# Optimization experiments

Measured on AMD Instinct MI355X. Metric: run time of the kernel, lower is better.

## Reference

```python
import jax, jax.numpy as jnp
import numpy as np
import math

N_SSM = 64
DIRECTIONS = 4

def setup_inputs() -> dict:
    key = jax.random.key(0)
    ks = jax.random.split(key, 10)
    S, B, E = 1024, 16, 1024
    H, N = DIRECTIONS * N_SSM, 2  # kernel_dim, ndim
    d = {}
    d['x'] = jax.random.normal(ks[0], (S, B, E), jnp.float32)
    for i, name in enumerate(['A_1', 'A_2', 'A_3', 'A_4']):
        d[name] = 0.2 * jax.random.normal(ks[1 + i], (H, N), jnp.float32)
    d['B_1'] = 0.2 * jax.random.normal(ks[5], (H, N), jnp.float32)
    d['B_2'] = 0.2 * jax.random.normal(ks[6], (H, N), jnp.float32)
    d['C_1'] = jax.random.normal(ks[7], (H, N), jnp.float32)
    d['C_2'] = jax.random.normal(ks[8], (H, N), jnp.float32)
    d['omega'] = jax.random.normal(ks[9], (E,), jnp.float32)
    return d


def _compute_kernel(A_1, A_2, A_3, A_4, B_1, B_2, C_1, C_2, Ls):
    # 2D SSM impulse response on an Ls x Ls grid (real, diagonal state dim N).
    # Recurrence (input = delta at (0,0)):
    #   x_h[i,j] = A1*x_h[i,j-1] + A2*x_v[i,j-1] + B1*u[i,j]
    #   x_v[i,j] = A3*x_h[i-1,j] + A4*x_v[i-1,j] + B2*u[i,j]
    #   k[i,j]   = scale*(C1.x_h[i,j] + C2.x_v[i,j])
    H, N = A_1.shape
    scale = math.sqrt(1.0 / N)
    A1, A2 = jax.nn.sigmoid(A_1), jax.nn.sigmoid(A_2)
    A3, A4 = jax.nn.sigmoid(A_3), jax.nn.sigmoid(A_4)
    B1, B2 = jax.nn.sigmoid(B_1), jax.nn.sigmoid(B_2)
    zeros_row = jnp.zeros((Ls, H, N), A1.dtype)

    def row_step(carry, i):
        xh_prev, xv_prev = carry  # [Ls, H, N] from row i-1
        first = (i == 0).astype(A1.dtype)
        xv_row = A3 * xh_prev + A4 * xv_prev
        xv_row = xv_row.at[0].add(first * B2)
        xv_shift = jnp.concatenate([jnp.zeros((1, H, N), A1.dtype), xv_row[:-1]], axis=0)
        c = A2 * xv_shift
        c = c.at[0].add(first * B1)

        def col_step(xh_left, cj):
            xh = A1 * xh_left + cj
            return xh, xh

        _, xh_row = jax.lax.scan(col_step, jnp.zeros((H, N), A1.dtype), c)
        y_row = scale * (jnp.einsum('lhn,hn->lh', xh_row, C_1)
                         + jnp.einsum('lhn,hn->lh', xv_row, C_2))
        return (xh_row, xv_row), y_row

    _, K = jax.lax.scan(row_step, (zeros_row, zeros_row), jnp.arange(Ls))  # [Ls, Ls, H]
    # boundary corrections from the original code
    K = K.at[0, :, :].multiply(2.0)
    K = K.at[:, 0, :].multiply(2.0)
    K = K.at[0, 0].divide(4.0)
    return K  # [Ls, Ls, H]


def _fft_conv2d(xd, kd, Ls):
    # xd: [B, E, Ls, Ls], kd: [E, Ls, Ls] -> linear 2D conv via zero-padded FFT
    s = (2 * Ls, 2 * Ls)
    kf = jnp.fft.rfft2(kd, s=s)          # [E, 2Ls, Ls+1]
    xf = jnp.fft.rfft2(xd, s=s)          # [B, E, 2Ls, Ls+1]
    y = jnp.fft.irfft2(xf * kf, s=s)
    return y[..., :Ls, :Ls]


def reference(x, A_1, A_2, A_3, A_4, B_1, B_2, C_1, C_2, omega):
    S, B, E = x.shape
    Ls = int(math.isqrt(S))
    H = C_1.shape[0]                      # kernel_dim = directions * n_ssm
    n_ssm = H // DIRECTIONS
    rep = E // n_ssm

    residual = x * omega                  # [S, B, E]
    x4 = x.transpose(1, 2, 0).reshape(B, E, Ls, Ls)

    K = _compute_kernel(A_1, A_2, A_3, A_4, B_1, B_2, C_1, C_2, Ls)  # [Ls, Ls, H]
    K = K.transpose(2, 0, 1)              # [H, Ls, Ls]

    flip_dims = [(), (-2,), (-1,), (-2, -1)]
    out = jnp.zeros_like(x4)
    for d, flips in enumerate(flip_dims):
        kd = jnp.tile(K[d * n_ssm:(d + 1) * n_ssm], (rep, 1, 1))  # [E, Ls, Ls]
        xd = jnp.flip(x4, axis=flips) if flips else x4
        y = _fft_conv2d(xd, kd, Ls)
        out = out + (jnp.flip(y, axis=flips) if flips else y)

    out = out.reshape(B, E, S).transpose(2, 0, 1)  # [S, B, E]
    return jax.nn.silu(out + residual)
```

## Files before the change

kernel.cpp:

```cpp
#include <hip/hip_runtime.h>
#include <hip/hip_fp16.h>


#define NPB 8
#define THREADS 256
#define M_TOT 16384
#define SCALE 0.70710678118654752f

typedef __attribute__((ext_vector_type(2))) float v2f;

__device__ __forceinline__ v2f v2s(float s) { return (v2f){s, s}; }
__device__ __forceinline__ v2f pfma(v2f a, v2f b, v2f c) {
    return __builtin_elementwise_fma(a, b, c);
}

template<int CTRL, int ROW_MASK, bool BC>
__device__ __forceinline__ float dppf(float v) {
    return __int_as_float(__builtin_amdgcn_update_dpp(
        0, __float_as_int(v), CTRL, ROW_MASK, 0xF, BC));
}
template<int CTRL, int ROW_MASK, bool BC>
__device__ __forceinline__ v2f dpp2(v2f v) {
    v2f r;
    r.x = dppf<CTRL, ROW_MASK, BC>(v.x);
    r.y = dppf<CTRL, ROW_MASK, BC>(v.y);
    return r;
}
__device__ __forceinline__ v2f swz2(v2f v) {
    v2f r;
    r.x = __int_as_float(__builtin_amdgcn_ds_swizzle(__float_as_int(v.x), 0x0200));
    r.y = __int_as_float(__builtin_amdgcn_ds_swizzle(__float_as_int(v.y), 0x0200));
    return r;
}

__device__ __forceinline__ float sigm(float v) { return 1.0f / (1.0f + __expf(-v)); }

struct DirP2 {
    v2f a1, p2, p4, p8, w;
    v2f a2z, ab, a3, a4, b1, b2, a3b1, c1s, c2s;
    float k00;
};

__device__ __forceinline__ v2f scanF2(v2f v, const DirP2& P) {
    v = pfma(P.a1, dpp2<0x111, 0xF, true >(v), v);
    v = pfma(P.p2, dpp2<0x112, 0xF, true >(v), v);
    v = pfma(P.p4, dpp2<0x114, 0xF, true >(v), v);
    v = pfma(P.p8, dpp2<0x118, 0xF, true >(v), v);
    v = pfma(P.w,  dpp2<0x142, 0xA, false>(v), v);
    return v;
}
__device__ __forceinline__ v2f scanR2(v2f v, const DirP2& P) {
    v = pfma(P.a1, dpp2<0x101, 0xF, true>(v), v);
    v = pfma(P.p2, dpp2<0x102, 0xF, true>(v), v);
    v = pfma(P.p4, dpp2<0x104, 0xF, true>(v), v);
    v = pfma(P.p8, dpp2<0x108, 0xF, true>(v), v);
    v = pfma(P.w,  swz2(v), v);
    return v;
}

template<bool REV>
__device__ __forceinline__ void dir_init2(DirP2& P, int h, int j,
    const float* __restrict__ A1p, const float* __restrict__ A2p,
    const float* __restrict__ A3p, const float* __restrict__ A4p,
    const float* __restrict__ B1p, const float* __restrict__ B2p,
    const float* __restrict__ C1p, const float* __restrict__ C2p)
{
    float2 a1r = *(const float2*)(A1p + 2 * h);
    float2 a2r = *(const float2*)(A2p + 2 * h);
    float2 a3r = *(const float2*)(A3p + 2 * h);
    float2 a4r = *(const float2*)(A4p + 2 * h);
    float2 b1r = *(const float2*)(B1p + 2 * h);
    float2 b2r = *(const float2*)(B2p + 2 * h);
    float2 c1r = *(const float2*)(C1p + 2 * h);
    float2 c2r = *(const float2*)(C2p + 2 * h);
    float a1v0 = sigm(a1r.x), a1v1 = sigm(a1r.y);
    P.a1 = (v2f){a1v0, a1v1};
    P.p2 = P.a1 * P.a1; P.p4 = P.p2 * P.p2; P.p8 = P.p4 * P.p4;
    P.a3 = (v2f){sigm(a3r.x), sigm(a3r.y)};
    P.a4 = (v2f){sigm(a4r.x), sigm(a4r.y)};
    P.b1 = (v2f){sigm(b1r.x), sigm(b1r.y)};
    P.b2 = (v2f){sigm(b2r.x), sigm(b2r.y)};
    P.a3b1 = P.a3 * P.b1;
    P.c1s = (v2f){SCALE * c1r.x, SCALE * c1r.y};
    P.c2s = (v2f){SCALE * c2r.x, SCALE * c2r.y};
    v2f kk = P.c1s * P.b1 + P.c2s * P.b2;
    P.k00 = kk.x + kk.y;
    const bool edge = REV ? (j == 31) : (j == 0);
    v2f a2n = (v2f){sigm(a2r.x), sigm(a2r.y)};
    P.a2z = edge ? (v2f){0.f, 0.f} : a2n;
    P.ab  = P.a2z * P.b2;
    if (REV) {
        if ((j & 16) == 0) {
            float e = (float)(16 - (j & 15));
            P.w = (v2f){__powf(a1v0, e), __powf(a1v1, e)};
        } else {
            P.w = (v2f){0.f, 0.f};
        }
    } else {
        float e = (float)((j & 15) + 1);
        P.w = (v2f){__powf(a1v0, e), __powf(a1v1, e)};
    }
}

template<bool REV>
__device__ __forceinline__ float dir_step2(const DirP2& P, v2f u2, v2f up2,
    v2f& xh, v2f& xv, v2f& cx)
{
    v2f b2u = P.b2 * u2;
    v2f nxv = pfma(P.a3, xh, pfma(P.a4, xv, b2u));
    v2f ncx = pfma(P.a3b1, up2, pfma(P.a4, cx, b2u));
    v2f xl, ul2;
    if constexpr (REV) {
        xl  = dpp2<0x130, 0xF, true>(nxv);
        ul2 = dpp2<0x130, 0xF, true>(u2);
    } else {
        xl  = dpp2<0x138, 0xF, true>(nxv);
        ul2 = dpp2<0x138, 0xF, true>(u2);
    }
    v2f b1u = P.b1 * u2;
    v2f d = pfma(P.a2z, xl, b1u);
    v2f e = pfma(P.ab, ul2, b1u);
    v2f nh, rh;
    if constexpr (REV) { nh = scanR2(d, P); rh = scanR2(e, P); }
    else               { nh = scanF2(d, P); rh = scanF2(e, P); }
    v2f acc = pfma(P.c1s, nh + rh, P.c2s * (nxv + ncx));
    xh = nh; xv = nxv; cx = ncx;
    return acc.x + acc.y;
}

__global__ __launch_bounds__(THREADS) void ssm2d_kernel(
    const float* __restrict__ x,
    const float* __restrict__ A1p, const float* __restrict__ A2p,
    const float* __restrict__ A3p, const float* __restrict__ A4p,
    const float* __restrict__ B1p, const float* __restrict__ B2p,
    const float* __restrict__ C1p, const float* __restrict__ C2p,
    const float* __restrict__ omega,
    float* __restrict__ out)
{
    __shared__ float  u_lds[NPB * 1024];
    __shared__ __half a_lds[NPB * 1024];
    const int t = threadIdx.x;
    const int bid = blockIdx.x;
    const int m0  = ((bid & 7) * 256 + (bid >> 3)) * NPB;

    const int simg = t & 7;
    #pragma unroll 4
    for (int it = 0; it < 32; ++it) {
        int pix = it * 32 + (t >> 3);
        u_lds[simg * 1024 + (pix ^ (simg << 2))] = x[(size_t)pix * M_TOT + (m0 + simg)];
    }
    __syncthreads();

    const int j    = t & 31;
    const int img  = t >> 5;
    const int m    = m0 + img;
    const int hb   = m & 63;
    const int colx = j ^ (img << 2);
    const float*  uim = u_lds + img * 1024;
    __half*       aim = a_lds + img * 1024;
    const float om = omega[m & 1023];

    {
        DirP2 P0, P2;
        dir_init2<false>(P0, hb,       j, A1p, A2p, A3p, A4p, B1p, B2p, C1p, C2p);
        dir_init2<true >(P2, 128 + hb, j, A1p, A2p, A3p, A4p, B1p, B2p, C1p, C2p);
        const float omA = om - P0.k00 - P2.k00;
        v2f xhA = {0,0}, xvA = {0,0}, cxA = {0,0};
        v2f xhB = {0,0}, xvB = {0,0}, cxB = {0,0};
        float up = 0.f;
        #pragma unroll 4
        for (int s = 0; s < 32; ++s) {
            float u  = uim[s * 32 + colx];
            v2f u2 = v2s(u), up2 = v2s(up);
            float y0 = dir_step2<false>(P0, u2, up2, xhA, xvA, cxA);
            float y2 = dir_step2<true >(P2, u2, up2, xhB, xvB, cxB);
            aim[s * 32 + colx] = __float2half(fmaf(u, omA, y0 + y2));
            up = u;
        }
    }
    {
        DirP2 P1, P3;
        dir_init2<false>(P1, 64 + hb,  j, A1p, A2p, A3p, A4p, B1p, B2p, C1p, C2p);
        dir_init2<true >(P3, 192 + hb, j, A1p, A2p, A3p, A4p, B1p, B2p, C1p, C2p);
        const float kB = P1.k00 + P3.k00;
        v2f xhA = {0,0}, xvA = {0,0}, cxA = {0,0};
        v2f xhB = {0,0}, xvB = {0,0}, cxB = {0,0};
        float up = 0.f;
        #pragma unroll 4
        for (int s = 0; s < 32; ++s) {
            int   r  = 31 - s;
            float u  = uim[r * 32 + colx];
            v2f u2 = v2s(u), up2 = v2s(up);
            float y1 = dir_step2<false>(P1, u2, up2, xhA, xvA, cxA);
            float y3 = dir_step2<true >(P3, u2, up2, xhB, xvB, cxB);
            float z  = __half2float(aim[r * 32 + colx]) + y1 + y3;
            z = fmaf(u, -kB, z);
            float sg = 1.0f / (1.0f + __expf(-z));
            aim[r * 32 + colx] = __float2half(z * sg);
            up = u;
        }
    }
    __syncthreads();

    #pragma unroll 4
    for (int it = 0; it < 32; ++it) {
        int pix = it * 32 + (t >> 3);
        out[(size_t)pix * M_TOT + (m0 + simg)] =
            __half2float(a_lds[simg * 1024 + (pix ^ (simg << 2))]);
    }
}

extern "C" void kernel_launch(void* const* d_in, const int* in_sizes, int n_in,
                              void* d_out, int out_size, void* d_ws, size_t ws_size,
                              hipStream_t stream) {
    const float* x  = (const float*)d_in[0];
    const float* A1 = (const float*)d_in[1];
    const float* A2 = (const float*)d_in[2];
    const float* A3 = (const float*)d_in[3];
    const float* A4 = (const float*)d_in[4];
    const float* B1 = (const float*)d_in[5];
    const float* B2 = (const float*)d_in[6];
    const float* C1 = (const float*)d_in[7];
    const float* C2 = (const float*)d_in[8];
    const float* om = (const float*)d_in[9];
    float* out = (float*)d_out;
    hipLaunchKernelGGL(ssm2d_kernel, dim3(M_TOT / NPB), dim3(THREADS), 0, stream,
                       x, A1, A2, A3, A4, B1, B2, C1, C2, om, out);
}
```

Baseline: 245.1 us.

## Run SSM recurrence in packed fp16 with fused DPP FMA scans

Converts the per-step state recurrence and parallel scans from packed fp32 to packed fp16, using inline-asm v_pk_fmac_f16_dpp to fuse each lane shift with its FMA. The reverse-direction scan is rewritten as a forward scan on column-mirrored input (colr) with a swizzle reversal of the output, so both directions share one forward DPP pattern. Input staging in LDS becomes fp16 and the output dot products use fdot2. This cuts VALU and DPP instruction count and register pressure, at the cost of fp16 rounding error building up over the 32-step recurrence.

Measured after the change: 210.7 us. 1.16x faster.

```diff
diff --git a/kernel.cpp b/kernel.cpp
--- a/kernel.cpp
+++ b/kernel.cpp
@@ -7,59 +7,34 @@
 #define M_TOT 16384
 #define SCALE 0.70710678118654752f
 
-typedef __attribute__((ext_vector_type(2))) float v2f;
-
-__device__ __forceinline__ v2f v2s(float s) { return (v2f){s, s}; }
-__device__ __forceinline__ v2f pfma(v2f a, v2f b, v2f c) {
+typedef __attribute__((ext_vector_type(2))) _Float16 v2h;
+
+__device__ __forceinline__ unsigned h2u(v2h v) { return __builtin_bit_cast(unsigned, v); }
+__device__ __forceinline__ v2h u2h(unsigned v) { return __builtin_bit_cast(v2h, v); }
+__device__ __forceinline__ v2h hfma2v(v2h a, v2h b, v2h c) {
     return __builtin_elementwise_fma(a, b, c);
 }
-
-template<int CTRL, int ROW_MASK, bool BC>
-__device__ __forceinline__ float dppf(float v) {
-    return __int_as_float(__builtin_amdgcn_update_dpp(
-        0, __float_as_int(v), CTRL, ROW_MASK, 0xF, BC));
-}
-template<int CTRL, int ROW_MASK, bool BC>
-__device__ __forceinline__ v2f dpp2(v2f v) {
-    v2f r;
-    r.x = dppf<CTRL, ROW_MASK, BC>(v.x);
-    r.y = dppf<CTRL, ROW_MASK, BC>(v.y);
-    return r;
-}
-__device__ __forceinline__ v2f swz2(v2f v) {
-    v2f r;
-    r.x = __int_as_float(__builtin_amdgcn_ds_swizzle(__float_as_int(v.x), 0x0200));
-    r.y = __int_as_float(__builtin_amdgcn_ds_swizzle(__float_as_int(v.y), 0x0200));
-    return r;
-}
-
+__device__ __forceinline__ v2h cvt2(float x, float y) {
+    return (v2h){(_Float16)x, (_Float16)y};
+}
+
+template<int CTRL>
+__device__ __forceinline__ v2h dpph(v2h v) {
+    return u2h((unsigned)__builtin_amdgcn_update_dpp(
+        0, (int)h2u(v), CTRL, 0xF, 0xF, true));
+}
+__device__ __forceinline__ float swzrev(float v) {
+    return __int_as_float(__builtin_amdgcn_ds_swizzle(__float_as_int(v), 0x7C1F));
+}
 __device__ __forceinline__ float sigm(float v) { return 1.0f / (1.0f + __expf(-v)); }
 
-struct DirP2 {
-    v2f a1, p2, p4, p8, w;
-    v2f a2z, ab, a3, a4, b1, b2, a3b1, c1s, c2s;
+struct DirPH {
+    v2h a1, p2, p4, p8, w;
+    v2h a2z, ab, a3, a4, b1, b2, a3b1, c1, c2;
     float k00;
 };
 
-__device__ __forceinline__ v2f scanF2(v2f v, const DirP2& P) {
-    v = pfma(P.a1, dpp2<0x111, 0xF, true >(v), v);
-    v = pfma(P.p2, dpp2<0x112, 0xF, true >(v), v);
-    v = pfma(P.p4, dpp2<0x114, 0xF, true >(v), v);
-    v = pfma(P.p8, dpp2<0x118, 0xF, true >(v), v);
-    v = pfma(P.w,  dpp2<0x142, 0xA, false>(v), v);
-    return v;
-}
-__device__ __forceinline__ v2f scanR2(v2f v, const DirP2& P) {
-    v = pfma(P.a1, dpp2<0x101, 0xF, true>(v), v);
-    v = pfma(P.p2, dpp2<0x102, 0xF, true>(v), v);
-    v = pfma(P.p4, dpp2<0x104, 0xF, true>(v), v);
-    v = pfma(P.p8, dpp2<0x108, 0xF, true>(v), v);
-    v = pfma(P.w,  swz2(v), v);
-    return v;
-}
-
-template<bool REV>
-__device__ __forceinline__ void dir_init2(DirP2& P, int h, int j,
+__device__ __forceinline__ void dir_init_h(DirPH& P, int h, int j,
     const float* __restrict__ A1p, const float* __restrict__ A2p,
     const float* __restrict__ A3p, const float* __restrict__ A4p,
     const float* __restrict__ B1p, const float* __restrict__ B2p,
@@ -74,58 +49,85 @@
     float2 c1r = *(const float2*)(C1p + 2 * h);
     float2 c2r = *(const float2*)(C2p + 2 * h);
     float a1v0 = sigm(a1r.x), a1v1 = sigm(a1r.y);
-    P.a1 = (v2f){a1v0, a1v1};
-    P.p2 = P.a1 * P.a1; P.p4 = P.p2 * P.p2; P.p8 = P.p4 * P.p4;
-    P.a3 = (v2f){sigm(a3r.x), sigm(a3r.y)};
-    P.a4 = (v2f){sigm(a4r.x), sigm(a4r.y)};
-    P.b1 = (v2f){sigm(b1r.x), sigm(b1r.y)};
-    P.b2 = (v2f){sigm(b2r.x), sigm(b2r.y)};
-    P.a3b1 = P.a3 * P.b1;
-    P.c1s = (v2f){SCALE * c1r.x, SCALE * c1r.y};
-    P.c2s = (v2f){SCALE * c2r.x, SCALE * c2r.y};
-    v2f kk = P.c1s * P.b1 + P.c2s * P.b2;
-    P.k00 = kk.x + kk.y;
-    const bool edge = REV ? (j == 31) : (j == 0);
-    v2f a2n = (v2f){sigm(a2r.x), sigm(a2r.y)};
-    P.a2z = edge ? (v2f){0.f, 0.f} : a2n;
-    P.ab  = P.a2z * P.b2;
-    if (REV) {
-        if ((j & 16) == 0) {
-            float e = (float)(16 - (j & 15));
-            P.w = (v2f){__powf(a1v0, e), __powf(a1v1, e)};
-        } else {
-            P.w = (v2f){0.f, 0.f};
-        }
-    } else {
-        float e = (float)((j & 15) + 1);
-        P.w = (v2f){__powf(a1v0, e), __powf(a1v1, e)};
-    }
-}
-
-template<bool REV>
-__device__ __forceinline__ float dir_step2(const DirP2& P, v2f u2, v2f up2,
-    v2f& xh, v2f& xv, v2f& cx)
-{
-    v2f b2u = P.b2 * u2;
-    v2f nxv = pfma(P.a3, xh, pfma(P.a4, xv, b2u));
-    v2f ncx = pfma(P.a3b1, up2, pfma(P.a4, cx, b2u));
-    v2f xl, ul2;
-    if constexpr (REV) {
-        xl  = dpp2<0x130, 0xF, true>(nxv);
-        ul2 = dpp2<0x130, 0xF, true>(u2);
-    } else {
-        xl  = dpp2<0x138, 0xF, true>(nxv);
-        ul2 = dpp2<0x138, 0xF, true>(u2);
-    }
-    v2f b1u = P.b1 * u2;
-    v2f d = pfma(P.a2z, xl, b1u);
-    v2f e = pfma(P.ab, ul2, b1u);
-    v2f nh, rh;
-    if constexpr (REV) { nh = scanR2(d, P); rh = scanR2(e, P); }
-    else               { nh = scanF2(d, P); rh = scanF2(e, P); }
-    v2f acc = pfma(P.c1s, nh + rh, P.c2s * (nxv + ncx));
+    float p2v0 = a1v0 * a1v0, p2v1 = a1v1 * a1v1;
+    float p4v0 = p2v0 * p2v0, p4v1 = p2v1 * p2v1;
+    float p8v0 = p4v0 * p4v0, p8v1 = p4v1 * p4v1;
+    float a3v0 = sigm(a3r.x), a3v1 = sigm(a3r.y);
+    float a4v0 = sigm(a4r.x), a4v1 = sigm(a4r.y);
+    float b1v0 = sigm(b1r.x), b1v1 = sigm(b1r.y);
+    float b2v0 = sigm(b2r.x), b2v1 = sigm(b2r.y);
+    float c1v0 = SCALE * c1r.x, c1v1 = SCALE * c1r.y;
+    float c2v0 = SCALE * c2r.x, c2v1 = SCALE * c2r.y;
+    P.a1 = cvt2(a1v0, a1v1); P.p2 = cvt2(p2v0, p2v1);
+    P.p4 = cvt2(p4v0, p4v1); P.p8 = cvt2(p8v0, p8v1);
+    P.a3 = cvt2(a3v0, a3v1); P.a4 = cvt2(a4v0, a4v1);
+    P.b1 = cvt2(b1v0, b1v1); P.b2 = cvt2(b2v0, b2v1);
+    P.a3b1 = cvt2(a3v0 * b1v0, a3v1 * b1v1);
+    P.c1 = cvt2(c1v0, c1v1); P.c2 = cvt2(c2v0, c2v1);
+    P.k00 = c1v0 * b1v0 + c1v1 * b1v1 + c2v0 * b2v0 + c2v1 * b2v1;
+    const bool edge = (j == 0);
+    float z0 = edge ? 0.f : sigm(a2r.x);
+    float z1 = edge ? 0.f : sigm(a2r.y);
+    P.a2z = cvt2(z0, z1);
+    P.ab  = cvt2(z0 * b2v0, z1 * b2v1);
+    float e = (float)((j & 15) + 1);
+    P.w = cvt2(__powf(a1v0, e), __powf(a1v1, e));
+}
+
+__device__ __forceinline__ void dir_pre_h(const DirPH& P, v2h u2, v2h up2,
+    v2h xh, v2h xv, v2h cx, v2h& nxv, v2h& ncx, v2h& d, v2h& e)
+{
+    v2h b2u = P.b2 * u2;
+    nxv = hfma2v(P.a3, xh, hfma2v(P.a4, xv, b2u));
+    ncx = hfma2v(P.a3b1, up2, hfma2v(P.a4, cx, b2u));
+    v2h xl = dpph<0x138>(nxv);
+    v2h ul = dpph<0x138>(u2);
+    v2h b1u = P.b1 * u2;
+    d = hfma2v(P.a2z, xl, b1u);
+    e = hfma2v(P.ab, ul, b1u);
+}
+
+__device__ __forceinline__ float dir_post_h(const DirPH& P, v2h nh, v2h rh,
+    v2h nxv, v2h ncx, v2h& xh, v2h& xv, v2h& cx, float base)
+{
+    v2h s1 = nh + rh;
+    v2h s2 = nxv + ncx;
+    float y = __builtin_amdgcn_fdot2(P.c1, s1,
+              __builtin_amdgcn_fdot2(P.c2, s2, base, false), false);
     xh = nh; xv = nxv; cx = ncx;
-    return acc.x + acc.y;
+    return y;
+}
+
+__device__ __forceinline__ void scan4h(
+    unsigned& f0, unsigned& f1, unsigned& r0, unsigned& r1,
+    const DirPH& PF, const DirPH& PR)
+{
+    asm("s_nop 1\n\t"
+        "v_pk_fmac_f16_dpp %0, %0, %4  row_shr:1 row_mask:0xf bank_mask:0xf bound_ctrl:0\n\t"
+        "v_pk_fmac_f16_dpp %1, %1, %4  row_shr:1 row_mask:0xf bank_mask:0xf bound_ctrl:0\n\t"
+        "v_pk_fmac_f16_dpp %2, %2, %9  row_shr:1 row_mask:0xf bank_mask:0xf bound_ctrl:0\n\t"
+        "v_pk_fmac_f16_dpp %3, %3, %9  row_shr:1 row_mask:0xf bank_mask:0xf bound_ctrl:0\n\t"
+        "v_pk_fmac_f16_dpp %0, %0, %5  row_shr:2 row_mask:0xf bank_mask:0xf bound_ctrl:0\n\t"
+        "v_pk_fmac_f16_dpp %1, %1, %5  row_shr:2 row_mask:0xf bank_mask:0xf bound_ctrl:0\n\t"
+        "v_pk_fmac_f16_dpp %2, %2, %10 row_shr:2 row_mask:0xf bank_mask:0xf bound_ctrl:0\n\t"
+        "v_pk_fmac_f16_dpp %3, %3, %10 row_shr:2 row_mask:0xf bank_mask:0xf bound_ctrl:0\n\t"
+        "v_pk_fmac_f16_dpp %0, %0, %6  row_shr:4 row_mask:0xf bank_mask:0xf bound_ctrl:0\n\t"
+        "v_pk_fmac_f16_dpp %1, %1, %6  row_shr:4 row_mask:0xf bank_mask:0xf bound_ctrl:0\n\t"
+        "v_pk_fmac_f16_dpp %2, %2, %11 row_shr:4 row_mask:0xf bank_mask:0xf bound_ctrl:0\n\t"
+        "v_pk_fmac_f16_dpp %3, %3, %11 row_shr:4 row_mask:0xf bank_mask:0xf bound_ctrl:0\n\t"
+        "v_pk_fmac_f16_dpp %0, %0, %7  row_shr:8 row_mask:0xf bank_mask:0xf bound_ctrl:0\n\t"
+        "v_pk_fmac_f16_dpp %1, %1, %7  row_shr:8 row_mask:0xf bank_mask:0xf bound_ctrl:0\n\t"
+        "v_pk_fmac_f16_dpp %2, %2, %12 row_shr:8 row_mask:0xf bank_mask:0xf bound_ctrl:0\n\t"
+        "v_pk_fmac_f16_dpp %3, %3, %12 row_shr:8 row_mask:0xf bank_mask:0xf bound_ctrl:0\n\t"
+        "v_pk_fmac_f16_dpp %0, %0, %8  row_bcast:15 row_mask:0xa bank_mask:0xf bound_ctrl:0\n\t"
+        "v_pk_fmac_f16_dpp %1, %1, %8  row_bcast:15 row_mask:0xa bank_mask:0xf bound_ctrl:0\n\t"
+        "v_pk_fmac_f16_dpp %2, %2, %13 row_bcast:15 row_mask:0xa bank_mask:0xf bound_ctrl:0\n\t"
+        "v_pk_fmac_f16_dpp %3, %3, %13 row_bcast:15 row_mask:0xa bank_mask:0xf bound_ctrl:0"
+        : "+v"(f0), "+v"(f1), "+v"(r0), "+v"(r1)
+        : "v"(h2u(PF.a1)), "v"(h2u(PF.p2)), "v"(h2u(PF.p4)),
+          "v"(h2u(PF.p8)), "v"(h2u(PF.w)),
+          "v"(h2u(PR.a1)), "v"(h2u(PR.p2)), "v"(h2u(PR.p4)),
+          "v"(h2u(PR.p8)), "v"(h2u(PR.w)));
 }
 
 __global__ __launch_bounds__(THREADS) void ssm2d_kernel(
@@ -137,8 +139,8 @@
     const float* __restrict__ omega,
     float* __restrict__ out)
 {
-    __shared__ float  u_lds[NPB * 1024];
-    __shared__ __half a_lds[NPB * 1024];
+    __shared__ _Float16 u_lds[NPB * 1024];
+    __shared__ _Float16 a_lds[NPB * 1024];
     const int t = threadIdx.x;
     const int bid = blockIdx.x;
     const int m0  = ((bid & 7) * 256 + (bid >> 3)) * NPB;
@@ -147,7 +149,8 @@
     #pragma unroll 4
     for (int it = 0; it < 32; ++it) {
         int pix = it * 32 + (t >> 3);
-        u_lds[simg * 1024 + (pix ^ (simg << 2))] = x[(size_t)pix * M_TOT + (m0 + simg)];
+        u_lds[simg * 1024 + (pix ^ (simg << 2))] =
+            (_Float16)x[(size_t)pix * M_TOT + (m0 + simg)];
     }
     __syncthreads();
 
@@ -156,48 +159,70 @@
     const int m    = m0 + img;
     const int hb   = m & 63;
     const int colx = j ^ (img << 2);
-    const float*  uim = u_lds + img * 1024;
-    __half*       aim = a_lds + img * 1024;
+    const int colr = 31 ^ colx;
+    const _Float16* uim = u_lds + img * 1024;
+    _Float16*       aim = a_lds + img * 1024;
     const float om = omega[m & 1023];
 
     {
-        DirP2 P0, P2;
-        dir_init2<false>(P0, hb,       j, A1p, A2p, A3p, A4p, B1p, B2p, C1p, C2p);
-        dir_init2<true >(P2, 128 + hb, j, A1p, A2p, A3p, A4p, B1p, B2p, C1p, C2p);
-        const float omA = om - P0.k00 - P2.k00;
-        v2f xhA = {0,0}, xvA = {0,0}, cxA = {0,0};
-        v2f xhB = {0,0}, xvB = {0,0}, cxB = {0,0};
-        float up = 0.f;
+        DirPH P0, P2;
+        dir_init_h(P0, hb,       j, A1p, A2p, A3p, A4p, B1p, B2p, C1p, C2p);
+        dir_init_h(P2, 128 + hb, j, A1p, A2p, A3p, A4p, B1p, B2p, C1p, C2p);
+        const float omA = om - P0.k00;
+        v2h xhF = {0,0}, xvF = {0,0}, cxF = {0,0};
+        v2h xhR = {0,0}, xvR = {0,0}, cxR = {0,0};
+        v2h up2 = {0,0}, upr2 = {0,0};
         #pragma unroll 4
         for (int s = 0; s < 32; ++s) {
-            float u  = uim[s * 32 + colx];
-            v2f u2 = v2s(u), up2 = v2s(up);
-            float y0 = dir_step2<false>(P0, u2, up2, xhA, xvA, cxA);
-            float y2 = dir_step2<true >(P2, u2, up2, xhB, xvB, cxB);
-            aim[s * 32 + colx] = __float2half(fmaf(u, omA, y0 + y2));
-            up = u;
+            _Float16 uh  = uim[s * 32 + colx];
+            _Float16 urh = uim[s * 32 + colr];
+            float uf = (float)uh, urf = (float)urh;
+            v2h u2  = (v2h){uh, uh};
+            v2h ur2 = (v2h){urh, urh};
+            v2h nxvF, ncxF, dF, eF, nxvR, ncxR, dR, eR;
+            dir_pre_h(P0, u2,  up2,  xhF, xvF, cxF, nxvF, ncxF, dF, eF);
+            dir_pre_h(P2, ur2, upr2, xhR, xvR, cxR, nxvR, ncxR, dR, eR);
+            unsigned f0 = h2u(dF), f1 = h2u(eF), r0 = h2u(dR), r1 = h2u(eR);
+            scan4h(f0, f1, r0, r1, P0, P2);
+            float y0 = dir_post_h(P0, u2h(f0), u2h(f1), nxvF, ncxF,
+                                  xhF, xvF, cxF, 0.f);
+            float y2 = dir_post_h(P2, u2h(r0), u2h(r1), nxvR, ncxR,
+                                  xhR, xvR, cxR, -P2.k00 * urf);
+            float y2f = swzrev(y2);
+            aim[s * 32 + colx] = (_Float16)fmaf(uf, omA, y0 + y2f);
+            up2 = u2; upr2 = ur2;
         }
     }
     {
-        DirP2 P1, P3;
-        dir_init2<false>(P1, 64 + hb,  j, A1p, A2p, A3p, A4p, B1p, B2p, C1p, C2p);
-        dir_init2<true >(P3, 192 + hb, j, A1p, A2p, A3p, A4p, B1p, B2p, C1p, C2p);
-        const float kB = P1.k00 + P3.k00;
-        v2f xhA = {0,0}, xvA = {0,0}, cxA = {0,0};
-        v2f xhB = {0,0}, xvB = {0,0}, cxB = {0,0};
-        float up = 0.f;
+        DirPH P1, P3;
+        dir_init_h(P1, 64 + hb,  j, A1p, A2p, A3p, A4p, B1p, B2p, C1p, C2p);
+        dir_init_h(P3, 192 + hb, j, A1p, A2p, A3p, A4p, B1p, B2p, C1p, C2p);
+        v2h xhF = {0,0}, xvF = {0,0}, cxF = {0,0};
+        v2h xhR = {0,0}, xvR = {0,0}, cxR = {0,0};
+        v2h up2 = {0,0}, upr2 = {0,0};
         #pragma unroll 4
         for (int s = 0; s < 32; ++s) {
-            int   r  = 31 - s;
-            float u  = uim[r * 32 + colx];
-            v2f u2 = v2s(u), up2 = v2s(up);
-            float y1 = dir_step2<false>(P1, u2, up2, xhA, xvA, cxA);
-            float y3 = dir_step2<true >(P3, u2, up2, xhB, xvB, cxB);
-            float z  = __half2float(aim[r * 32 + colx]) + y1 + y3;
-            z = fmaf(u, -kB, z);
+            int   r   = 31 - s;
+            _Float16 uh  = uim[r * 32 + colx];
+            _Float16 urh = uim[r * 32 + colr];
+            float uf = (float)uh, urf = (float)urh;
+            v2h u2  = (v2h){uh, uh};
+            v2h ur2 = (v2h){urh, urh};
+            v2h nxvF, ncxF, dF, eF, nxvR, ncxR, dR, eR;
+            dir_pre_h(P1, u2,  up2,  xhF, xvF, cxF, nxvF, ncxF, dF, eF);
+            dir_pre_h(P3, ur2, upr2, xhR, xvR, cxR, nxvR, ncxR, dR, eR);
+            unsigned f0 = h2u(dF), f1 = h2u(eF), r0 = h2u(dR), r1 = h2u(eR);
+            scan4h(f0, f1, r0, r1, P1, P3);
+            float y1 = dir_post_h(P1, u2h(f0), u2h(f1), nxvF, ncxF,
+                                  xhF, xvF, cxF, 0.f);
+            float y3 = dir_post_h(P3, u2h(r0), u2h(r1), nxvR, ncxR,
+                                  xhR, xvR, cxR, -P3.k00 * urf);
+            float y3f = swzrev(y3);
+            float z  = (float)aim[r * 32 + colx] + y1 + y3f;
+            z = fmaf(uf, -P1.k00, z);
             float sg = 1.0f / (1.0f + __expf(-z));
-            aim[r * 32 + colx] = __float2half(z * sg);
-            up = u;
+            aim[r * 32 + colx] = (_Float16)(z * sg);
+            up2 = u2; upr2 = ur2;
         }
     }
     __syncthreads();
@@ -206,7 +231,7 @@
     for (int it = 0; it < 32; ++it) {
         int pix = it * 32 + (t >> 3);
         out[(size_t)pix * M_TOT + (m0 + simg)] =
-            __half2float(a_lds[simg * 1024 + (pix ^ (simg << 2))]);
+            (float)a_lds[simg * 1024 + (pix ^ (simg << 2))];
     }
 }
 
```
